# Optimization experiments

Hardware: AMD Instinct MI355X
Metric: run time of the kernel (lower is better)

The kernel has to match this reference:

```python
import jax, jax.numpy as jnp
import numpy as np

R_MIN = 0.1
R_MAX = 2.0

B, N, K = 8, 8192, 100  # batch, atoms, max neighbors


def setup_inputs() -> dict:
    key = jax.random.key(0)
    k1, k2, k3, k4, k5 = jax.random.split(key, 5)
    positions = jax.random.normal(k1, (B, N, 3), dtype=jnp.float32)
    cell = jax.random.normal(k2, (B, 3, 3), dtype=jnp.float32)
    offsets = jax.random.normal(k3, (B, N, K, 3), dtype=jnp.float32)
    neighbors = jax.random.randint(k4, (B, N, K), 0, N, dtype=jnp.int64)
    mask = jax.random.randint(k5, (B, N, K), 0, 2, dtype=jnp.int32)
    return {"positions": positions, "cell": cell, "offsets": offsets,
            "neighbors": neighbors, "mask": mask}


def reference(positions, cell, offsets, neighbors, mask):
    # gather neighbor positions: [B, N, K, 3]
    pos_j = jax.vmap(lambda p, n: p[n])(positions, neighbors)
    # fractional offsets -> cartesian: offsets @ cell per batch
    pos_j = pos_j + jnp.einsum('bnkd,bdc->bnkc', offsets, cell)
    vec = pos_j - positions[:, :, None, :]          # [B, N, K, 3]
    sq = jnp.sum(vec * vec, axis=-1)                # [B, N, K]
    valid = mask > 0
    sq_safe = jnp.where(valid, sq, 1.0)
    d = jnp.where(valid, jnp.sqrt(sq_safe), 0.0)    # masked distances = 0
    # f = 1/d^2, zeroed where d < r_min or d > r_max (masked entries have d=0 < r_min)
    keep = (d >= R_MIN) & (d <= R_MAX)
    f = jnp.where(keep, 1.0 / sq_safe, 0.0)
    return jnp.sum(f, axis=(1, 2)) * 0.5            # [B]
```

## Files before the change

### kernel.cpp

```cpp
#include <hip/hip_runtime.h>

typedef int   __attribute__((ext_vector_type(4))) i32x4;
typedef float __attribute__((ext_vector_type(4))) f32x4;

constexpr int B_ = 8;
constexpr int N_ = 8192;
constexpr int K_ = 100;
constexpr int PER_BATCH = N_ * K_;
constexpr int QUADS_PER_BATCH = PER_BATCH / 4;
constexpr int THREADS = 1024;
constexpr int BLOCKS_PER_BATCH = 32;
constexpr int GRID = B_ * BLOCKS_PER_BATCH;
constexpr int QUADS_PER_BLOCK = QUADS_PER_BATCH / BLOCKS_PER_BATCH;
constexpr int FULL_ITERS = QUADS_PER_BLOCK / THREADS;
constexpr int TAIL = QUADS_PER_BLOCK - FULL_ITERS * THREADS;

constexpr float RMIN2 = 0.01f;
constexpr float RMAX2 = 4.0f;

__global__ __launch_bounds__(THREADS, 1)
void repulsive_prior_kernel(const float* __restrict__ positions,
                            const float* __restrict__ cell,
                            const float* __restrict__ offsets,
                            const int*   __restrict__ neighbors,
                            const int*   __restrict__ mask,
                            float* __restrict__ out)
{
    __shared__ f32x4 spos[N_];
    __shared__ float wsum[THREADS / 64];

    const int bid   = blockIdx.x;
    const int b     = bid >> 5;
    const int chunk = bid & 31;
    const int t     = (int)threadIdx.x;

    const float* __restrict__ pos_b = positions + (size_t)b * N_ * 3;
    const float* __restrict__ off_b = offsets   + (size_t)b * PER_BATCH * 3;
    const int*   __restrict__ nb_b  = neighbors + (size_t)b * PER_BATCH;
    const int*   __restrict__ mk_b  = mask      + (size_t)b * PER_BATCH;

    const int qbase = chunk * QUADS_PER_BLOCK;
    auto qat = [&](int k) { return qbase + k * THREADS + t; };

    struct Quad { i32x4 nb, mk; f32x4 oa, ob, oc; };
    auto loadq = [&](int q) {
        Quad Q;
        Q.nb = *(const i32x4*)(nb_b  + 4 * (size_t)q);
        Q.mk = *(const i32x4*)(mk_b  + 4 * (size_t)q);
        Q.oa = *(const f32x4*)(off_b + 12 * (size_t)q);
        Q.ob = *(const f32x4*)(off_b + 12 * (size_t)q + 4);
        Q.oc = *(const f32x4*)(off_b + 12 * (size_t)q + 8);
        return Q;
    };

    Quad Q0 = loadq(qat(0));
    Quad Q1 = loadq(qat(1));
    Quad Q2 = loadq(qat(2));

    #pragma unroll
    for (int g0 = 0; g0 < 2; ++g0) {
        const int g = g0 * THREADS + t;
        const f32x4 v0 = *(const f32x4*)(pos_b + 12 * (size_t)g);
        const f32x4 v1 = *(const f32x4*)(pos_b + 12 * (size_t)g + 4);
        const f32x4 v2 = *(const f32x4*)(pos_b + 12 * (size_t)g + 8);
        f32x4 r0; r0.x = v0.x; r0.y = v0.y; r0.z = v0.z; r0.w = 0.0f;
        f32x4 r1; r1.x = v0.w; r1.y = v1.x; r1.z = v1.y; r1.w = 0.0f;
        f32x4 r2; r2.x = v1.z; r2.y = v1.w; r2.z = v2.x; r2.w = 0.0f;
        f32x4 r3; r3.x = v2.y; r3.y = v2.z; r3.z = v2.w; r3.w = 0.0f;
        spos[4 * g + 0] = r0;
        spos[4 * g + 1] = r1;
        spos[4 * g + 2] = r2;
        spos[4 * g + 3] = r3;
    }
    __syncthreads();

    const float* cb = cell + b * 9;
    const float c00 = cb[0], c01 = cb[1], c02 = cb[2];
    const float c10 = cb[3], c11 = cb[4], c12 = cb[5];
    const float c20 = cb[6], c21 = cb[7], c22 = cb[8];

    float acc = 0.0f;
    auto computeq = [&](const Quad& Q, int q) {
        const int n = q / 25;
        const f32x4 pi = spos[n];
        auto elem = [&](int m, int j, float o0, float o1, float o2) {
            const f32x4 pj = spos[j];
            const float vx = pj.x + o0 * c00 + o1 * c10 + o2 * c20 - pi.x;
            const float vy = pj.y + o0 * c01 + o1 * c11 + o2 * c21 - pi.y;
            const float vz = pj.z + o0 * c02 + o1 * c12 + o2 * c22 - pi.z;
            const float sq = vx * vx + vy * vy + vz * vz;
            const bool keep = (m > 0) & (sq >= RMIN2) & (sq <= RMAX2);
            acc += keep ? (1.0f / sq) : 0.0f;
        };
        elem(Q.mk.x, Q.nb.x, Q.oa.x, Q.oa.y, Q.oa.z);
        elem(Q.mk.y, Q.nb.y, Q.oa.w, Q.ob.x, Q.ob.y);
        elem(Q.mk.z, Q.nb.z, Q.ob.z, Q.ob.w, Q.oc.x);
        elem(Q.mk.w, Q.nb.w, Q.oc.y, Q.oc.z, Q.oc.w);
    };

    Q0 = Q0;
    {
        Quad Q3 = loadq(qat(3));
        computeq(Q0, qat(0));
        Quad Q4 = loadq(qat(4));
        computeq(Q1, qat(1));
        Quad Q5 = loadq(qat(5));
        computeq(Q2, qat(2));
        const bool hastail = t < TAIL;
        if (hastail) {
            Quad Q6 = loadq(qat(6));
            computeq(Q3, qat(3));
            computeq(Q4, qat(4));
            computeq(Q5, qat(5));
            computeq(Q6, qat(6));
        } else {
            computeq(Q3, qat(3));
            computeq(Q4, qat(4));
            computeq(Q5, qat(5));
        }
    }

    #pragma unroll
    for (int off = 32; off > 0; off >>= 1)
        acc += __shfl_down(acc, off, 64);

    const int wave = t >> 6;
    const int lane = t & 63;
    if (lane == 0) wsum[wave] = acc;
    __syncthreads();
    if (t == 0) {
        float s = 0.0f;
        #pragma unroll
        for (int w = 0; w < THREADS / 64; ++w) s += wsum[w];
        atomicAdd(&out[b], 0.5f * s);
    }
}

extern "C" void kernel_launch(void* const* d_in, const int* in_sizes, int n_in,
                              void* d_out, int out_size, void* d_ws, size_t ws_size,
                              hipStream_t stream) {
    const float* positions = (const float*)d_in[0];
    const float* cell      = (const float*)d_in[1];
    const float* offsets   = (const float*)d_in[2];
    const int*   neighbors = (const int*)d_in[3];
    const int*   mask      = (const int*)d_in[4];
    float* out = (float*)d_out;

    (void)hipMemsetAsync(out, 0, out_size * sizeof(float), stream);

    repulsive_prior_kernel<<<GRID, THREADS, 0, stream>>>(
        positions, cell, offsets, neighbors, mask, out);
}
```

Measured before the change: 32.34 us.

## Pack shared positions as fp16 to fit two blocks per CU, doubling grid

Neighbor positions in LDS are stored as three fp16 values in 8 bytes instead of an fp32 float4. This halves the shared footprint so two 1024-thread blocks can be resident per CU, and the grid doubles to 64 blocks per batch, interleaved across batches. The goal is better latency hiding for a mostly bandwidth-bound gather. The cost is that every block still stages the whole position table, so redundant staging doubles, and fp16 rounding of positions may shift results near the cutoff radii and affect tolerance.

```diff
diff --git a/kernel.cpp b/kernel.cpp
--- a/kernel.cpp
+++ b/kernel.cpp
@@ -1,7 +1,9 @@
 #include <hip/hip_runtime.h>
+#include <hip/hip_fp16.h>
 
-typedef int   __attribute__((ext_vector_type(4))) i32x4;
-typedef float __attribute__((ext_vector_type(4))) f32x4;
+typedef int            __attribute__((ext_vector_type(4))) i32x4;
+typedef float          __attribute__((ext_vector_type(4))) f32x4;
+typedef unsigned int   __attribute__((ext_vector_type(2))) u32x2;
 
 constexpr int B_ = 8;
 constexpr int N_ = 8192;
@@ -9,7 +11,7 @@
 constexpr int PER_BATCH = N_ * K_;
 constexpr int QUADS_PER_BATCH = PER_BATCH / 4;
 constexpr int THREADS = 1024;
-constexpr int BLOCKS_PER_BATCH = 32;
+constexpr int BLOCKS_PER_BATCH = 64;
 constexpr int GRID = B_ * BLOCKS_PER_BATCH;
 constexpr int QUADS_PER_BLOCK = QUADS_PER_BATCH / BLOCKS_PER_BATCH;
 constexpr int FULL_ITERS = QUADS_PER_BLOCK / THREADS;
@@ -18,7 +20,15 @@
 constexpr float RMIN2 = 0.01f;
 constexpr float RMAX2 = 4.0f;
 
-__global__ __launch_bounds__(THREADS, 1)
+__device__ __forceinline__ u32x2 pack_pos(float x, float y, float z) {
+    const unsigned hx = __half_as_ushort(__float2half_rn(x));
+    const unsigned hy = __half_as_ushort(__float2half_rn(y));
+    const unsigned hz = __half_as_ushort(__float2half_rn(z));
+    u32x2 r; r.x = hx | (hy << 16); r.y = hz;
+    return r;
+}
+
+__global__ __launch_bounds__(THREADS, 2)
 void repulsive_prior_kernel(const float* __restrict__ positions,
                             const float* __restrict__ cell,
                             const float* __restrict__ offsets,
@@ -26,12 +36,12 @@
                             const int*   __restrict__ mask,
                             float* __restrict__ out)
 {
-    __shared__ f32x4 spos[N_];
+    __shared__ u32x2 spos[N_];
     __shared__ float wsum[THREADS / 64];
 
     const int bid   = blockIdx.x;
-    const int b     = bid >> 5;
-    const int chunk = bid & 31;
+    const int b     = bid & 7;
+    const int chunk = bid >> 3;
     const int t     = (int)threadIdx.x;
 
     const float* __restrict__ pos_b = positions + (size_t)b * N_ * 3;
@@ -54,8 +64,6 @@
     };
 
     Quad Q0 = loadq(qat(0));
-    Quad Q1 = loadq(qat(1));
-    Quad Q2 = loadq(qat(2));
 
     #pragma unroll
     for (int g0 = 0; g0 < 2; ++g0) {
@@ -63,14 +71,10 @@
         const f32x4 v0 = *(const f32x4*)(pos_b + 12 * (size_t)g);
         const f32x4 v1 = *(const f32x4*)(pos_b + 12 * (size_t)g + 4);
         const f32x4 v2 = *(const f32x4*)(pos_b + 12 * (size_t)g + 8);
-        f32x4 r0; r0.x = v0.x; r0.y = v0.y; r0.z = v0.z; r0.w = 0.0f;
-        f32x4 r1; r1.x = v0.w; r1.y = v1.x; r1.z = v1.y; r1.w = 0.0f;
-        f32x4 r2; r2.x = v1.z; r2.y = v1.w; r2.z = v2.x; r2.w = 0.0f;
-        f32x4 r3; r3.x = v2.y; r3.y = v2.z; r3.z = v2.w; r3.w = 0.0f;
-        spos[4 * g + 0] = r0;
-        spos[4 * g + 1] = r1;
-        spos[4 * g + 2] = r2;
-        spos[4 * g + 3] = r3;
+        spos[4 * g + 0] = pack_pos(v0.x, v0.y, v0.z);
+        spos[4 * g + 1] = pack_pos(v0.w, v1.x, v1.y);
+        spos[4 * g + 2] = pack_pos(v1.z, v1.w, v2.x);
+        spos[4 * g + 3] = pack_pos(v2.y, v2.z, v2.w);
     }
     __syncthreads();
 
@@ -79,15 +83,24 @@
     const float c10 = cb[3], c11 = cb[4], c12 = cb[5];
     const float c20 = cb[6], c21 = cb[7], c22 = cb[8];
 
+    auto ldpos = [&](int row, float& x, float& y, float& z) {
+        const u32x2 v = spos[row];
+        x = __half2float(__ushort_as_half((unsigned short)(v.x & 0xffffu)));
+        y = __half2float(__ushort_as_half((unsigned short)(v.x >> 16)));
+        z = __half2float(__ushort_as_half((unsigned short)(v.y & 0xffffu)));
+    };
+
     float acc = 0.0f;
     auto computeq = [&](const Quad& Q, int q) {
         const int n = q / 25;
-        const f32x4 pi = spos[n];
+        float pix, piy, piz;
+        ldpos(n, pix, piy, piz);
         auto elem = [&](int m, int j, float o0, float o1, float o2) {
-            const f32x4 pj = spos[j];
-            const float vx = pj.x + o0 * c00 + o1 * c10 + o2 * c20 - pi.x;
-            const float vy = pj.y + o0 * c01 + o1 * c11 + o2 * c21 - pi.y;
-            const float vz = pj.z + o0 * c02 + o1 * c12 + o2 * c22 - pi.z;
+            float pjx, pjy, pjz;
+            ldpos(j, pjx, pjy, pjz);
+            const float vx = pjx + o0 * c00 + o1 * c10 + o2 * c20 - pix;
+            const float vy = pjy + o0 * c01 + o1 * c11 + o2 * c21 - piy;
+            const float vz = pjz + o0 * c02 + o1 * c12 + o2 * c22 - piz;
             const float sq = vx * vx + vy * vy + vz * vz;
             const bool keep = (m > 0) & (sq >= RMIN2) & (sq <= RMAX2);
             acc += keep ? (1.0f / sq) : 0.0f;
@@ -98,26 +111,16 @@
         elem(Q.mk.w, Q.nb.w, Q.oc.y, Q.oc.z, Q.oc.w);
     };
 
-    Q0 = Q0;
-    {
-        Quad Q3 = loadq(qat(3));
-        computeq(Q0, qat(0));
-        Quad Q4 = loadq(qat(4));
-        computeq(Q1, qat(1));
-        Quad Q5 = loadq(qat(5));
+    Quad Q1 = loadq(qat(1));
+    computeq(Q0, qat(0));
+    Quad Q2 = loadq(qat(2));
+    computeq(Q1, qat(1));
+    if (t < TAIL) {
+        Quad QT = loadq(qat(3));
         computeq(Q2, qat(2));
-        const bool hastail = t < TAIL;
-        if (hastail) {
-            Quad Q6 = loadq(qat(6));
-            computeq(Q3, qat(3));
-            computeq(Q4, qat(4));
-            computeq(Q5, qat(5));
-            computeq(Q6, qat(6));
-        } else {
-            computeq(Q3, qat(3));
-            computeq(Q4, qat(4));
-            computeq(Q5, qat(5));
-        }
+        computeq(QT, qat(3));
+    } else {
+        computeq(Q2, qat(2));
     }
 
     #pragma unroll
```

Result: faster. 31.49 us (-2.6%).
